# Performance work log

Hardware: AMD Instinct MI355X
Metric: run time of the kernel (lower is better)

The kernel has to match this reference:

```python
import jax, jax.numpy as jnp
import numpy as np

B, S, D, H = 4, 2048, 1024, 16
HD = D // H


def setup_inputs() -> dict:
    key = jax.random.key(0)
    ks = jax.random.split(key, 5)
    scale = 1.0 / np.sqrt(D)
    return {
        "x": jax.random.normal(ks[0], (B, S, D), dtype=jnp.float32),
        "W_q": jax.random.normal(ks[1], (D, D), dtype=jnp.float32) * scale,
        "W_k": jax.random.normal(ks[2], (D, D), dtype=jnp.float32) * scale,
        "W_v": jax.random.normal(ks[3], (D, D), dtype=jnp.float32) * scale,
        "W_o": jax.random.normal(ks[4], (D, D), dtype=jnp.float32) * scale,
    }


def reference(x, W_q, W_k, W_v, W_o):
    b, s, d = x.shape
    # fused QKV projections; reshape to per-head layout [b, s, H, HD]
    q = (x @ W_q).reshape(b, s, H, HD)
    k = (x @ W_k).reshape(b, s, H, HD)
    v = (x @ W_v).reshape(b, s, H, HD)
    # scaled dot-product scores [b, H, s, s]
    scores = jnp.einsum("bqhd,bkhd->bhqk", q, k) / jnp.sqrt(jnp.asarray(HD, x.dtype))
    # causal mask: disallow attending to future positions (j > i)
    causal = jnp.tril(jnp.ones((s, s), dtype=bool))
    scores = jnp.where(causal[None, None], scores, jnp.finfo(x.dtype).min)
    attn = jax.nn.softmax(scores, axis=-1)
    # attention output back to [b, s, d], then output projection (W_o applied as x @ W_o.T)
    out = jnp.einsum("bhqk,bkhd->bqhd", attn, v).reshape(b, s, d)
    return out @ W_o.T
```

## Files before the change

kernel.cpp:

```cpp
#include <hip/hip_runtime.h>
#include <hip/hip_bf16.h>
#include <stdint.h>

#define B_  4
#define S_  2048
#define D_  1024
#define H_  16
#define HD_ 64
#define M_  (B_*S_)

typedef __bf16 bf16_t;
typedef __bf16 bf16x8 __attribute__((ext_vector_type(8)));
typedef __bf16 bf16x4 __attribute__((ext_vector_type(4)));
typedef __bf16 bf16x2 __attribute__((ext_vector_type(2)));
typedef float  f32x4  __attribute__((ext_vector_type(4)));
typedef unsigned int uint2v __attribute__((ext_vector_type(2)));

#define EXP2(x) __builtin_amdgcn_exp2f(x)
#define CS_ 0.18033688011112042f

__global__ void cvt_f32_to_bf16(const float* __restrict__ src, bf16_t* __restrict__ dst, int n) {
  int stride = gridDim.x * blockDim.x * 4;
  for (int i = (blockIdx.x * blockDim.x + threadIdx.x) * 4; i < n; i += stride) {
    float4 v = *(const float4*)(src + i);
    bf16x4 o = { (bf16_t)v.x, (bf16_t)v.y, (bf16_t)v.z, (bf16_t)v.w };
    *(bf16x4*)(dst + i) = o;
  }
}

__global__ void cvt_transpose_w(const float* __restrict__ wq, const float* __restrict__ wk,
                                const float* __restrict__ wv, const float* __restrict__ wof,
                                bf16_t* __restrict__ dst, bf16_t* __restrict__ wob) {
  __shared__ float t[32][33];
  int w = blockIdx.z;
  int c0 = blockIdx.x * 32, r0 = blockIdx.y * 32;
  int tx = threadIdx.x, ty = threadIdx.y;
  if (w == 3) {
#pragma unroll
    for (int i = 0; i < 4; i++)
      wob[(size_t)(r0 + ty + i * 8) * D_ + c0 + tx] =
          (bf16_t)wof[(size_t)(r0 + ty + i * 8) * D_ + c0 + tx];
    return;
  }
  const float* src = (w == 0) ? wq : (w == 1) ? wk : wv;
  const float scl = (w == 0) ? CS_ : 1.0f;
#pragma unroll
  for (int i = 0; i < 4; i++)
    t[ty + i * 8][tx] = src[(size_t)(r0 + ty + i * 8) * D_ + c0 + tx];
  __syncthreads();
#pragma unroll
  for (int i = 0; i < 4; i++)
    dst[(size_t)(w * D_ + c0 + ty + i * 8) * D_ + r0 + tx] = (bf16_t)(t[tx][ty + i * 8] * scl);
}

template <typename OutT>
__global__ void gemm_nt(const bf16_t* __restrict__ A, const bf16_t* __restrict__ Bt,
                        OutT* __restrict__ C, int Mt, int N, int K) {
  __shared__ bf16_t As[128 * 64];
  __shared__ bf16_t Bs[128 * 64];
  const int bn = blockIdx.x, bm = blockIdx.y;
  const int tid = threadIdx.x;
  const int wv = tid >> 6, lane = tid & 63;
  const int wr = wv >> 1, wc = wv & 1;
  const int g = lane >> 4, r16 = lane & 15;
  const int m0 = bm * 128, n0 = bn * 128;

  f32x4 acc[4][4] = {};

  for (int kt = 0; kt < K; kt += 64) {
#pragma unroll
    for (int c = 0; c < 4; c++) {
      int ch = wv * 4 + c;
      int o = ch * 1024 + lane * 16;
      int row = o >> 7;
      int c16 = (o >> 4) & 7;
      const bf16_t* gA = A + (size_t)(m0 + row) * K + kt + ((c16 ^ (row & 7)) * 8);
      __builtin_amdgcn_global_load_lds((const __attribute__((address_space(1))) void*)gA,
          (__attribute__((address_space(3))) void*)((char*)As + ch * 1024), 16, 0, 0);
    }
#pragma unroll
    for (int c = 0; c < 4; c++) {
      int ch = wv * 4 + c;
      int o = ch * 1024 + lane * 16;
      int row = o >> 7;
      int c16 = (o >> 4) & 7;
      const bf16_t* gB = Bt + (size_t)(n0 + row) * K + kt + ((c16 ^ (row & 7)) * 8);
      __builtin_amdgcn_global_load_lds((const __attribute__((address_space(1))) void*)gB,
          (__attribute__((address_space(3))) void*)((char*)Bs + ch * 1024), 16, 0, 0);
    }
    __syncthreads();

#pragma unroll
    for (int kk = 0; kk < 2; kk++) {
      bf16x8 af[4], bfv[4];
#pragma unroll
      for (int i = 0; i < 4; i++) {
        int row = wr * 64 + i * 16 + r16;
        af[i] = *(const bf16x8*)((char*)As + row * 128 + (((kk * 4 + g) ^ (row & 7)) * 16));
      }
#pragma unroll
      for (int j = 0; j < 4; j++) {
        int row = wc * 64 + j * 16 + r16;
        bfv[j] = *(const bf16x8*)((char*)Bs + row * 128 + (((kk * 4 + g) ^ (row & 7)) * 16));
      }
#pragma unroll
      for (int i = 0; i < 4; i++)
#pragma unroll
        for (int j = 0; j < 4; j++)
          acc[i][j] = __builtin_amdgcn_mfma_f32_16x16x32_bf16(af[i], bfv[j], acc[i][j], 0, 0, 0);
    }
    __syncthreads();
  }

#pragma unroll
  for (int i = 0; i < 4; i++)
#pragma unroll
    for (int j = 0; j < 4; j++)
#pragma unroll
      for (int rr = 0; rr < 4; rr++) {
        int grow = m0 + wr * 64 + i * 16 + g * 4 + rr;
        int gcol = n0 + wc * 64 + j * 16 + r16;
        C[(size_t)grow * N + gcol] = (OutT)acc[i][j][rr];
      }
}

__global__ __launch_bounds__(256, 3) void attn_kernel(const bf16_t* __restrict__ QKV,
                                                      bf16_t* __restrict__ AO) {
  const int bh = blockIdx.x;
  const int y = (int)blockIdx.y;
  const int jj = y >> 2, gq = y & 3;
  const int qt = (jj == 0) ? (15 - gq) : (jj == 1) ? (8 + gq) : (jj == 2) ? (7 - gq) : gq;
  const int b = bh >> 4, h = bh & 15;
  const int tid = threadIdx.x, wv = tid >> 6, lane = tid & 63;
  const int g = lane >> 4, r16 = lane & 15;

  __shared__ bf16_t Ks[2][64 * 64];
  __shared__ bf16_t Vt[2][64 * 64];

  const size_t rowbase = (size_t)b * S_;
  const bf16_t* Qg = QKV + (rowbase + qt * 128) * 3072 + h * HD_;
  const bf16_t* Kg = QKV + rowbase * 3072 + 1024 + h * HD_;
  const bf16_t* Vg = QKV + rowbase * 3072 + 2048 + h * HD_;

  bf16x8 qf[2][2];
#pragma unroll
  for (int rg = 0; rg < 2; rg++) {
    int row = wv * 32 + rg * 16 + r16;
    const bf16_t* p = Qg + (size_t)row * 3072;
    qf[rg][0] = *(const bf16x8*)(p + g * 8);
    qf[rg][1] = *(const bf16x8*)(p + 32 + g * 8);
  }

  f32x4 o_acc[2][4] = {};
  float lrow[2] = {0.f, 0.f};

  int base_row[2];
  base_row[0] = qt * 128 + wv * 32;
  base_row[1] = base_row[0] + 16;

  const int kp0 = tid >> 4, dq = tid & 15;
  bf16x4 va0, vb0, va1, vb1;

  auto issueK = [&](int t, int buf) {
    const int kv0 = t * 64;
#pragma unroll
    for (int c = 0; c < 2; c++) {
      int chunkid = wv * 2 + c;
      int o = chunkid * 1024 + lane * 16;
      int row = o >> 7;
      int ch = (o >> 4) & 7;
      const bf16_t* src = Kg + (size_t)(kv0 + row) * 3072 + ((ch ^ (row & 7)) * 8);
      __builtin_amdgcn_global_load_lds((const __attribute__((address_space(1))) void*)src,
          (__attribute__((address_space(3))) void*)((char*)(&Ks[buf][0]) + chunkid * 1024), 16, 0, 0);
    }
  };
  auto loadV = [&](int t) {
    const int kv0 = t * 64;
    const bf16_t* p0 = Vg + (size_t)(kv0 + kp0 * 2) * 3072 + dq * 4;
    va0 = *(const bf16x4*)p0;
    vb0 = *(const bf16x4*)(p0 + 3072);
    const bf16_t* p1 = Vg + (size_t)(kv0 + (16 + kp0) * 2) * 3072 + dq * 4;
    va1 = *(const bf16x4*)p1;
    vb1 = *(const bf16x4*)(p1 + 3072);
  };
  auto writeV = [&](int buf) {
#pragma unroll
    for (int j = 0; j < 4; j++) {
      int d = dq * 4 + j;
      int sz = (((d & 7) ^ (d >> 3)) << 2);
      bf16x2 q0 = { va0[j], vb0[j] };
      *(bf16x2*)(&Vt[buf][d * 64 + (kp0 ^ sz) * 2]) = q0;
      bf16x2 q1 = { va1[j], vb1[j] };
      *(bf16x2*)(&Vt[buf][d * 64 + ((16 + kp0) ^ sz) * 2]) = q1;
    }
  };

  issueK(0, 0);
  loadV(0);

  const int ntiles = 2 * qt + 2;
  for (int t = 0; t < ntiles; t++) {
    const int cur = t & 1;
    const int kv0 = t * 64;

    asm volatile("s_waitcnt vmcnt(0)" ::: "memory");
    writeV(cur);
    __syncthreads();
    if (t + 1 < ntiles) { issueK(t + 1, cur ^ 1); loadV(t + 1); }

    bool skip[2], needmask[2];
#pragma unroll
    for (int rg = 0; rg < 2; rg++) {
      skip[rg] = kv0 > base_row[rg] + 15;
      needmask[rg] = (kv0 + 63) > base_row[rg];
    }

    f32x4 st[2][4];
    __builtin_amdgcn_s_setprio(1);
#pragma unroll
    for (int sub = 0; sub < 4; sub++) {
      int krow = sub * 16 + r16;
      bf16x8 k0 = *(const bf16x8*)((char*)(&Ks[cur][0]) + krow * 128 + ((g ^ (krow & 7)) * 16));
      bf16x8 k1 = *(const bf16x8*)((char*)(&Ks[cur][0]) + krow * 128 + (((4 + g) ^ (krow & 7)) * 16));
#pragma unroll
      for (int rg = 0; rg < 2; rg++) {
        if (skip[rg]) continue;
        if (kv0 + sub * 16 > base_row[rg] + 15) {
          f32x4 ninf = { -1e30f, -1e30f, -1e30f, -1e30f };
          st[rg][sub] = ninf;
          continue;
        }
        f32x4 z = {};
        z = __builtin_amdgcn_mfma_f32_16x16x32_bf16(k0, qf[rg][0], z, 0, 0, 0);
        z = __builtin_amdgcn_mfma_f32_16x16x32_bf16(k1, qf[rg][1], z, 0, 0, 0);
        st[rg][sub] = z;
      }
    }
    __builtin_amdgcn_s_setprio(0);

    bf16x8 pf[2][2];
#pragma unroll
    for (int rg = 0; rg < 2; rg++) {
      if (skip[rg]) continue;
      const int qrow = base_row[rg] + r16;
      if (needmask[rg]) {
#pragma unroll
        for (int sub = 0; sub < 4; sub++)
#pragma unroll
          for (int rr = 0; rr < 4; rr++)
            if (kv0 + sub * 16 + g * 4 + rr > qrow) st[rg][sub][rr] = -1e30f;
      }
      float lsum = 0.f;
      unsigned int W[4][2];
#pragma unroll
      for (int sub = 0; sub < 4; sub++)
#pragma unroll
        for (int rrp = 0; rrp < 2; rrp++) {
          float p0 = EXP2(st[rg][sub][2 * rrp]);
          float p1 = EXP2(st[rg][sub][2 * rrp + 1]);
          lsum += p0 + p1;
          bf16x2 pp = { (bf16_t)p0, (bf16_t)p1 };
          W[sub][rrp] = *(unsigned int*)&pp;
        }
      lrow[rg] += lsum;
      unsigned int pfw[2][4];
#pragma unroll
      for (int k2 = 0; k2 < 2; k2++)
#pragma unroll
        for (int rrp = 0; rrp < 2; rrp++) {
          uint2v xy = __builtin_amdgcn_permlane32_swap(W[2 * k2][rrp], W[2 * k2 + 1][rrp],
                                                       false, false);
          uint2v zw = __builtin_amdgcn_permlane16_swap(xy[0], xy[1], false, false);
          pfw[k2][rrp]     = zw[0];
          pfw[k2][2 + rrp] = zw[1];
        }
#pragma unroll
      for (int kh = 0; kh < 2; kh++) {
        union { unsigned int u[4]; bf16x8 v8; } U;
        U.u[0] = pfw[kh][0]; U.u[1] = pfw[kh][1];
        U.u[2] = pfw[kh][2]; U.u[3] = pfw[kh][3];
        pf[rg][kh] = U.v8;
      }
    }

    __builtin_amdgcn_s_setprio(1);
#pragma unroll
    for (int kh = 0; kh < 2; kh++) {
#pragma unroll
      for (int c = 0; c < 4; c++) {
        int d = c * 16 + r16;
        int wstart = (kh * 16 + g * 4) ^ (((d & 7) ^ (d >> 3)) << 2);
        bf16x8 vf = *(const bf16x8*)(&Vt[cur][d * 64 + wstart * 2]);
#pragma unroll
        for (int rg = 0; rg < 2; rg++) {
          if (skip[rg]) continue;
          o_acc[rg][c] = __builtin_amdgcn_mfma_f32_16x16x32_bf16(vf, pf[rg][kh], o_acc[rg][c], 0, 0, 0);
        }
      }
    }
    __builtin_amdgcn_s_setprio(0);
  }

#pragma unroll
  for (int rg = 0; rg < 2; rg++) {
    float v = lrow[rg];
    v += __shfl_xor(v, 16);
    v += __shfl_xor(v, 32);
    float linv = 1.0f / v;
    const size_t grow = rowbase + base_row[rg] + r16;
#pragma unroll
    for (int c = 0; c < 4; c++) {
      bf16x4 o = { (bf16_t)(o_acc[rg][c][0] * linv), (bf16_t)(o_acc[rg][c][1] * linv),
                   (bf16_t)(o_acc[rg][c][2] * linv), (bf16_t)(o_acc[rg][c][3] * linv) };
      *(bf16x4*)(&AO[grow * D_ + h * HD_ + c * 16 + g * 4]) = o;
    }
  }
}

extern "C" void kernel_launch(void* const* d_in, const int* in_sizes, int n_in,
                              void* d_out, int out_size, void* d_ws, size_t ws_size,
                              hipStream_t stream) {
  const float* x  = (const float*)d_in[0];
  const float* Wq = (const float*)d_in[1];
  const float* Wk = (const float*)d_in[2];
  const float* Wv = (const float*)d_in[3];
  const float* Wo = (const float*)d_in[4];
  float* out = (float*)d_out;

  char* ws = (char*)d_ws;
  bf16_t* xb   = (bf16_t*)(ws);
  bf16_t* wqkv = (bf16_t*)(ws + 16777216);
  bf16_t* wo   = (bf16_t*)(ws + 16777216 + 6291456);
  bf16_t* qkv  = (bf16_t*)(ws + 25165824);
  bf16_t* ao   = (bf16_t*)(ws + 75497472);

  cvt_f32_to_bf16<<<1024, 256, 0, stream>>>(x, xb, M_ * D_);
  cvt_transpose_w<<<dim3(32, 32, 4), dim3(32, 8), 0, stream>>>(Wq, Wk, Wv, Wo, wqkv, wo);

  gemm_nt<bf16_t><<<dim3(3072 / 128, M_ / 128), 256, 0, stream>>>(xb, wqkv, qkv, M_, 3072, D_);

  attn_kernel<<<dim3(B_ * H_, 16), 256, 0, stream>>>(qkv, ao);

  gemm_nt<float><<<dim3(D_ / 128, M_ / 128), 256, 0, stream>>>(ao, wo, out, M_, D_, D_);
}
```

Measured before the change: 168.5 us.

## Halve attention query tile to 64 rows and double grid blocks

The attention kernel now gives each block 64 query rows, one 16-row group per wave, instead of 128 rows, and launches 32 query tiles per batch-head. Blocks are ordered heaviest-first (qt = 31 - blockIdx.y), replacing the interleaved causal load-balancing map. This aims to raise parallelism and even out the causal triangle's uneven work across blocks. In exchange, each loaded K/V tile is reused by half as many query rows, so K/V traffic and LDS staging per unit of work roughly double.

Result: no change. 171.4 us (+1.7%).

```diff
diff --git a/kernel.cpp b/kernel.cpp
--- a/kernel.cpp
+++ b/kernel.cpp
@@ -127,9 +127,7 @@
 __global__ __launch_bounds__(256, 3) void attn_kernel(const bf16_t* __restrict__ QKV,
                                                       bf16_t* __restrict__ AO) {
   const int bh = blockIdx.x;
-  const int y = (int)blockIdx.y;
-  const int jj = y >> 2, gq = y & 3;
-  const int qt = (jj == 0) ? (15 - gq) : (jj == 1) ? (8 + gq) : (jj == 2) ? (7 - gq) : gq;
+  const int qt = 31 - (int)blockIdx.y;
   const int b = bh >> 4, h = bh & 15;
   const int tid = threadIdx.x, wv = tid >> 6, lane = tid & 63;
   const int g = lane >> 4, r16 = lane & 15;
@@ -138,25 +136,21 @@
   __shared__ bf16_t Vt[2][64 * 64];
 
   const size_t rowbase = (size_t)b * S_;
-  const bf16_t* Qg = QKV + (rowbase + qt * 128) * 3072 + h * HD_;
+  const bf16_t* Qg = QKV + (rowbase + qt * 64) * 3072 + h * HD_;
   const bf16_t* Kg = QKV + rowbase * 3072 + 1024 + h * HD_;
   const bf16_t* Vg = QKV + rowbase * 3072 + 2048 + h * HD_;
 
-  bf16x8 qf[2][2];
-#pragma unroll
-  for (int rg = 0; rg < 2; rg++) {
-    int row = wv * 32 + rg * 16 + r16;
+  bf16x8 qf0, qf1;
+  {
+    int row = wv * 16 + r16;
     const bf16_t* p = Qg + (size_t)row * 3072;
-    qf[rg][0] = *(const bf16x8*)(p + g * 8);
-    qf[rg][1] = *(const bf16x8*)(p + 32 + g * 8);
-  }
-
-  f32x4 o_acc[2][4] = {};
-  float lrow[2] = {0.f, 0.f};
-
-  int base_row[2];
-  base_row[0] = qt * 128 + wv * 32;
-  base_row[1] = base_row[0] + 16;
+    qf0 = *(const bf16x8*)(p + g * 8);
+    qf1 = *(const bf16x8*)(p + 32 + g * 8);
+  }
+
+  f32x4 o_acc[4] = {};
+  float lrow = 0.f;
+  const int base_row = qt * 64 + wv * 16;
 
   const int kp0 = tid >> 4, dq = tid & 15;
   bf16x4 va0, vb0, va1, vb1;
@@ -198,7 +192,7 @@
   issueK(0, 0);
   loadV(0);
 
-  const int ntiles = 2 * qt + 2;
+  const int ntiles = qt + 1;
   for (int t = 0; t < ntiles; t++) {
     const int cur = t & 1;
     const int kv0 = t * 64;
@@ -208,47 +202,36 @@
     __syncthreads();
     if (t + 1 < ntiles) { issueK(t + 1, cur ^ 1); loadV(t + 1); }
 
-    bool skip[2], needmask[2];
-#pragma unroll
-    for (int rg = 0; rg < 2; rg++) {
-      skip[rg] = kv0 > base_row[rg] + 15;
-      needmask[rg] = (kv0 + 63) > base_row[rg];
-    }
-
-    f32x4 st[2][4];
-    __builtin_amdgcn_s_setprio(1);
-#pragma unroll
-    for (int sub = 0; sub < 4; sub++) {
-      int krow = sub * 16 + r16;
-      bf16x8 k0 = *(const bf16x8*)((char*)(&Ks[cur][0]) + krow * 128 + ((g ^ (krow & 7)) * 16));
-      bf16x8 k1 = *(const bf16x8*)((char*)(&Ks[cur][0]) + krow * 128 + (((4 + g) ^ (krow & 7)) * 16));
-#pragma unroll
-      for (int rg = 0; rg < 2; rg++) {
-        if (skip[rg]) continue;
-        if (kv0 + sub * 16 > base_row[rg] + 15) {
+    const bool skip = kv0 > base_row + 15;
+    const bool needmask = (kv0 + 63) > base_row;
+
+    f32x4 st[4];
+    if (!skip) {
+      __builtin_amdgcn_s_setprio(1);
+#pragma unroll
+      for (int sub = 0; sub < 4; sub++) {
+        int krow = sub * 16 + r16;
+        bf16x8 k0 = *(const bf16x8*)((char*)(&Ks[cur][0]) + krow * 128 + ((g ^ (krow & 7)) * 16));
+        bf16x8 k1 = *(const bf16x8*)((char*)(&Ks[cur][0]) + krow * 128 + (((4 + g) ^ (krow & 7)) * 16));
+        if (kv0 + sub * 16 > base_row + 15) {
           f32x4 ninf = { -1e30f, -1e30f, -1e30f, -1e30f };
-          st[rg][sub] = ninf;
+          st[sub] = ninf;
           continue;
         }
         f32x4 z = {};
-        z = __builtin_amdgcn_mfma_f32_16x16x32_bf16(k0, qf[rg][0], z, 0, 0, 0);
-        z = __builtin_amdgcn_mfma_f32_16x16x32_bf16(k1, qf[rg][1], z, 0, 0, 0);
-        st[rg][sub] = z;
-      }
-    }
-    __builtin_amdgcn_s_setprio(0);
-
-    bf16x8 pf[2][2];
-#pragma unroll
-    for (int rg = 0; rg < 2; rg++) {
-      if (skip[rg]) continue;
-      const int qrow = base_row[rg] + r16;
-      if (needmask[rg]) {
+        z = __builtin_amdgcn_mfma_f32_16x16x32_bf16(k0, qf0, z, 0, 0, 0);
+        z = __builtin_amdgcn_mfma_f32_16x16x32_bf16(k1, qf1, z, 0, 0, 0);
+        st[sub] = z;
+      }
+      __builtin_amdgcn_s_setprio(0);
+
+      const int qrow = base_row + r16;
+      if (needmask) {
 #pragma unroll
         for (int sub = 0; sub < 4; sub++)
 #pragma unroll
           for (int rr = 0; rr < 4; rr++)
-            if (kv0 + sub * 16 + g * 4 + rr > qrow) st[rg][sub][rr] = -1e30f;
+            if (kv0 + sub * 16 + g * 4 + rr > qrow) st[sub][rr] = -1e30f;
       }
       float lsum = 0.f;
       unsigned int W[4][2];
@@ -256,13 +239,13 @@
       for (int sub = 0; sub < 4; sub++)
 #pragma unroll
         for (int rrp = 0; rrp < 2; rrp++) {
-          float p0 = EXP2(st[rg][sub][2 * rrp]);
-          float p1 = EXP2(st[rg][sub][2 * rrp + 1]);
+          float p0 = EXP2(st[sub][2 * rrp]);
+          float p1 = EXP2(st[sub][2 * rrp + 1]);
           lsum += p0 + p1;
           bf16x2 pp = { (bf16_t)p0, (bf16_t)p1 };
           W[sub][rrp] = *(unsigned int*)&pp;
         }
-      lrow[rg] += lsum;
+      lrow += lsum;
       unsigned int pfw[2][4];
 #pragma unroll
       for (int k2 = 0; k2 < 2; k2++)
@@ -274,44 +257,40 @@
           pfw[k2][rrp]     = zw[0];
           pfw[k2][2 + rrp] = zw[1];
         }
+      bf16x8 pf[2];
 #pragma unroll
       for (int kh = 0; kh < 2; kh++) {
         union { unsigned int u[4]; bf16x8 v8; } U;
         U.u[0] = pfw[kh][0]; U.u[1] = pfw[kh][1];
         U.u[2] = pfw[kh][2]; U.u[3] = pfw[kh][3];
-        pf[rg][kh] = U.v8;
-      }
-    }
-
-    __builtin_amdgcn_s_setprio(1);
-#pragma unroll
-    for (int kh = 0; kh < 2; kh++) {
-#pragma unroll
-      for (int c = 0; c < 4; c++) {
-        int d = c * 16 + r16;
-        int wstart = (kh * 16 + g * 4) ^ (((d & 7) ^ (d >> 3)) << 2);
-        bf16x8 vf = *(const bf16x8*)(&Vt[cur][d * 64 + wstart * 2]);
-#pragma unroll
-        for (int rg = 0; rg < 2; rg++) {
-          if (skip[rg]) continue;
-          o_acc[rg][c] = __builtin_amdgcn_mfma_f32_16x16x32_bf16(vf, pf[rg][kh], o_acc[rg][c], 0, 0, 0);
+        pf[kh] = U.v8;
+      }
+
+      __builtin_amdgcn_s_setprio(1);
+#pragma unroll
+      for (int kh = 0; kh < 2; kh++) {
+#pragma unroll
+        for (int c = 0; c < 4; c++) {
+          int d = c * 16 + r16;
+          int wstart = (kh * 16 + g * 4) ^ (((d & 7) ^ (d >> 3)) << 2);
+          bf16x8 vf = *(const bf16x8*)(&Vt[cur][d * 64 + wstart * 2]);
+          o_acc[c] = __builtin_amdgcn_mfma_f32_16x16x32_bf16(vf, pf[kh], o_acc[c], 0, 0, 0);
         }
       }
-    }
-    __builtin_amdgcn_s_setprio(0);
-  }
-
-#pragma unroll
-  for (int rg = 0; rg < 2; rg++) {
-    float v = lrow[rg];
+      __builtin_amdgcn_s_setprio(0);
+    }
+  }
+
+  {
+    float v = lrow;
     v += __shfl_xor(v, 16);
     v += __shfl_xor(v, 32);
     float linv = 1.0f / v;
-    const size_t grow = rowbase + base_row[rg] + r16;
+    const size_t grow = rowbase + base_row + r16;
 #pragma unroll
     for (int c = 0; c < 4; c++) {
-      bf16x4 o = { (bf16_t)(o_acc[rg][c][0] * linv), (bf16_t)(o_acc[rg][c][1] * linv),
-                   (bf16_t)(o_acc[rg][c][2] * linv), (bf16_t)(o_acc[rg][c][3] * linv) };
+      bf16x4 o = { (bf16_t)(o_acc[c][0] * linv), (bf16_t)(o_acc[c][1] * linv),
+                   (bf16_t)(o_acc[c][2] * linv), (bf16_t)(o_acc[c][3] * linv) };
       *(bf16x4*)(&AO[grow * D_ + h * HD_ + c * 16 + g * 4]) = o;
     }
   }
@@ -339,7 +318,7 @@
 
   gemm_nt<bf16_t><<<dim3(3072 / 128, M_ / 128), 256, 0, stream>>>(xb, wqkv, qkv, M_, 3072, D_);
 
-  attn_kernel<<<dim3(B_ * H_, 16), 256, 0, stream>>>(qkv, ao);
+  attn_kernel<<<dim3(B_ * H_, 32), 256, 0, stream>>>(qkv, ao);
 
   gemm_nt<float><<<dim3(D_ / 128, M_ / 128), 256, 0, stream>>>(ao, wo, out, M_, D_, D_);
 }
```
